# Performance work log

Hardware: AMD Instinct MI355X
Metric: run time of the kernel (lower is better)

The kernel has to match this reference:

```python
import jax, jax.numpy as jnp
import numpy as np
import math

NUM_Q_HEADS = 32
NUM_KV_HEADS = 8


def setup_inputs() -> dict:
    key = jax.random.key(0)
    k1, k2, k3 = jax.random.split(key, 3)
    B, S, E = 2, 2048, 2048
    kv_E = NUM_KV_HEADS * (E // NUM_Q_HEADS)  # 512
    q = jax.random.normal(k1, (B, S, E), dtype=jnp.float32)
    k = jax.random.normal(k2, (B, S, kv_E), dtype=jnp.float32)
    v = jax.random.normal(k3, (B, S, kv_E), dtype=jnp.float32)
    return {"q": q, "k": k, "v": v}


def reference(q, k, v):
    B, S, E = q.shape
    H, KV = NUM_Q_HEADS, NUM_KV_HEADS
    D = E // H
    G = H // KV  # query heads per kv head
    scale = math.sqrt(D)
    # q heads laid out so group g of kv-head h corresponds to q-head h*G+g,
    # matching torch repeat_interleave semantics.
    qh = q.reshape(B, S, KV, G, D).transpose(0, 2, 3, 1, 4)  # [B,KV,G,S,D]
    kh = k.reshape(B, S, KV, D).transpose(0, 2, 1, 3)        # [B,KV,S,D]
    vh = v.reshape(B, S, KV, D).transpose(0, 2, 1, 3)        # [B,KV,S,D]
    scores = jnp.einsum('bkgsd,bktd->bkgst', qh, kh) / scale  # [B,KV,G,S,S]
    weights = jax.nn.softmax(scores, axis=-1)
    out = jnp.einsum('bkgst,bktd->bkgsd', weights, vh)        # [B,KV,G,S,D]
    # back to [B,S,E] with head order (kv_head, group) == q-head index
    return out.transpose(0, 3, 1, 2, 4).reshape(B, S, E)
```

## Files before the change

kernel.cpp:

```cpp
#include <hip/hip_runtime.h>
#include <hip/hip_bf16.h>


#define S_LEN 2048
#define E_DIM 2048
#define KV_E  512
#define D_HEAD 64
#define BN 64
#define NTILE (S_LEN / BN)

typedef __attribute__((ext_vector_type(8))) short short8;
typedef __attribute__((ext_vector_type(4))) float floatx4;

__device__ __forceinline__ short bf(float x) {
    return __builtin_bit_cast(short, __float2bfloat16(x));
}

__global__ __launch_bounds__(256)
void gqa_prepack_kernel(const float* __restrict__ k, const float* __restrict__ v,
                        short* __restrict__ ws) {
    __shared__ float kf[BN][D_HEAD + 2];
    __shared__ float vf[BN][D_HEAD + 2];
    const int kt = blockIdx.x, kvh = blockIdx.y, b = blockIdx.z;
    const int tid = threadIdx.x;
    short* wt = ws + ((size_t)(b * 8 + kvh) * NTILE + kt) * 8192;
    const float* kb = k + ((size_t)(b * S_LEN + kt * BN)) * KV_E + kvh * D_HEAD;
    const float* vb = v + ((size_t)(b * S_LEN + kt * BN)) * KV_E + kvh * D_HEAD;

    #pragma unroll
    for (int i = tid; i < 1024; i += 256) {
        const int r = i >> 4, c0 = (i & 15) << 2;
        floatx4 k4 = *((const floatx4*)(kb + (size_t)r * KV_E + c0));
        floatx4 v4 = *((const floatx4*)(vb + (size_t)r * KV_E + c0));
        kf[r][c0] = k4[0]; kf[r][c0 + 1] = k4[1]; kf[r][c0 + 2] = k4[2]; kf[r][c0 + 3] = k4[3];
        vf[r][c0] = v4[0]; vf[r][c0 + 1] = v4[1]; vf[r][c0 + 2] = v4[2]; vf[r][c0 + 3] = v4[3];
    }
    __syncthreads();
    #pragma unroll
    for (int c = tid; c < 1024; c += 256) {
        const int fk = c >> 6, l = c & 63;
        const int quad = l >> 4, lc = l & 15;
        const int ks = (fk >> 2) & 1, sub = fk & 3;
        short8 s;
        if (fk < 8) {
            const int row = ((lc >> 2) << 3) + (lc & 3) + ((sub & 1) << 2) + ((sub >> 1) << 5);
            const int c0 = ks * 32 + quad * 8;
            #pragma unroll
            for (int j = 0; j < 8; ++j) s[j] = bf(kf[row][c0 + j]);
        } else {
            const int d = sub * 16 + lc;
            const int k0 = ks * 32 + quad * 8;
            #pragma unroll
            for (int j = 0; j < 8; ++j) s[j] = bf(vf[k0 + j][d]);
        }
        *((short8*)(wt + c * 8)) = s;
    }
}

__global__ __launch_bounds__(256, 4)
void GroupedQueryAttention_36163624632989_kernel(
        const float* __restrict__ q,
        const short* __restrict__ ws,
        float* __restrict__ out, const int B) {
    __shared__ short lds[2 * 8192];

    const int f = blockIdx.x;
    const int chunk = gridDim.x >> 3;
    const int wg = (f & 7) * chunk + (f >> 3);
    const int qt = wg & 31;
    const int t2 = wg >> 5;
    const int b  = t2 % B;
    const int hp = t2 / B;
    const int kvh = hp >> 1;

    const int tid  = threadIdx.x;
    const int w    = tid >> 6;
    const int lane = tid & 63;
    const int quad = lane >> 4;
    const int lc   = lane & 15;

    const int h = (hp << 1) + (w & 1);
    const int rowhalf = w >> 1;

    const float SCL = 1.4426950408889634f / 8.0f;

    const short ONE = (short)0x3F80;
    const short8 ones8 = {ONE, ONE, ONE, ONE, ONE, ONE, ONE, ONE};

    short8 aq[2][2];
    #pragma unroll
    for (int mt = 0; mt < 2; ++mt) {
        const int qrow = qt * 64 + rowhalf * 32 + mt * 16 + lc;
        const float* qp = q + ((size_t)(b * S_LEN + qrow)) * E_DIM + h * D_HEAD;
        #pragma unroll
        for (int ks = 0; ks < 2; ++ks) {
            const float* p = qp + ks * 32 + quad * 8;
            floatx4 qa = *((const floatx4*)p);
            floatx4 qb = *((const floatx4*)(p + 4));
            aq[mt][ks][0] = bf(qa[0] * SCL); aq[mt][ks][1] = bf(qa[1] * SCL);
            aq[mt][ks][2] = bf(qa[2] * SCL); aq[mt][ks][3] = bf(qa[3] * SCL);
            aq[mt][ks][4] = bf(qb[0] * SCL); aq[mt][ks][5] = bf(qb[1] * SCL);
            aq[mt][ks][6] = bf(qb[2] * SCL); aq[mt][ks][7] = bf(qb[3] * SCL);
        }
    }

    floatx4 o_acc[2][4];
    floatx4 accL[2];
    #pragma unroll
    for (int mt = 0; mt < 2; ++mt) {
        accL[mt] = (floatx4){0.f, 0.f, 0.f, 0.f};
        #pragma unroll
        for (int i = 0; i < 4; ++i)
            o_acc[mt][i] = (floatx4){0.f, 0.f, 0.f, 0.f};
    }

    const short* wsT = ws + (size_t)(b * 8 + kvh) * NTILE * 8192;

    auto stage = [&](int buf, int kt) {
        const short* src = wsT + (size_t)kt * 8192 + w * 2048 + (lane << 3);
        short* dst = lds + buf * 8192 + w * 2048;
        #pragma unroll
        for (int i = 0; i < 4; ++i)
            __builtin_amdgcn_global_load_lds(
                (const __attribute__((address_space(1))) void*)(src + i * 512),
                (__attribute__((address_space(3))) void*)(dst + i * 512),
                16, 0, 0);
    };

    stage(0, 0);
    __syncthreads();
    int cur = 0;

    for (int kt = 0; kt < NTILE; ++kt) {
        if (kt + 1 < NTILE) stage(cur ^ 1, kt + 1);

        const short* fb = lds + cur * 8192 + (lane << 3);

        floatx4 accT[2][4];
        #pragma unroll
        for (int mt = 0; mt < 2; ++mt)
            #pragma unroll
            for (int t = 0; t < 4; ++t)
                accT[mt][t] = (floatx4){0.f, 0.f, 0.f, 0.f};
        #pragma unroll
        for (int ks = 0; ks < 2; ++ks) {
            short8 bk4[4];
            #pragma unroll
            for (int t = 0; t < 4; ++t)
                bk4[t] = *((const short8*)(fb + (ks * 4 + t) * 512));
            #pragma unroll
            for (int mt = 0; mt < 2; ++mt)
                #pragma unroll
                for (int t = 0; t < 4; ++t)
                    accT[mt][t] = __builtin_amdgcn_mfma_f32_16x16x32_bf16(
                        bk4[t], aq[mt][ks], accT[mt][t], 0, 0, 0);
        }

        #pragma unroll
        for (int ks = 0; ks < 2; ++ks) {
            short8 bv4[4];
            #pragma unroll
            for (int nt = 0; nt < 4; ++nt)
                bv4[nt] = *((const short8*)(fb + (8 + ks * 4 + nt) * 512));
            #pragma unroll
            for (int mt = 0; mt < 2; ++mt) {
                short8 ap;
                #pragma unroll
                for (int r = 0; r < 4; ++r) {
                    ap[r]     = bf(__builtin_amdgcn_exp2f(accT[mt][2 * ks][r]));
                    ap[4 + r] = bf(__builtin_amdgcn_exp2f(accT[mt][2 * ks + 1][r]));
                }
                #pragma unroll
                for (int nt = 0; nt < 4; ++nt)
                    o_acc[mt][nt] = __builtin_amdgcn_mfma_f32_16x16x32_bf16(
                        ap, bv4[nt], o_acc[mt][nt], 0, 0, 0);
                accL[mt] = __builtin_amdgcn_mfma_f32_16x16x32_bf16(
                    ap, ones8, accL[mt], 0, 0, 0);
            }
        }

        __syncthreads();
        cur ^= 1;
    }

    #pragma unroll
    for (int mt = 0; mt < 2; ++mt) {
        float* op = out + (size_t)b * S_LEN * E_DIM + h * D_HEAD;
        #pragma unroll
        for (int r = 0; r < 4; ++r) {
            const float inv_l = 1.0f / accL[mt][r];
            const int grow = qt * 64 + rowhalf * 32 + mt * 16 + quad * 4 + r;
            #pragma unroll
            for (int nt = 0; nt < 4; ++nt)
                op[(size_t)grow * E_DIM + nt * 16 + lc] = o_acc[mt][nt][r] * inv_l;
        }
    }
}

extern "C" void kernel_launch(void* const* d_in, const int* in_sizes, int n_in,
                              void* d_out, int out_size, void* d_ws, size_t ws_size,
                              hipStream_t stream) {
    const float* q = (const float*)d_in[0];
    const float* k = (const float*)d_in[1];
    const float* v = (const float*)d_in[2];
    float* out = (float*)d_out;
    short* ws = (short*)d_ws;
    const int B = in_sizes[0] / (S_LEN * E_DIM);

    dim3 pgrid(NTILE, 8, B);
    gqa_prepack_kernel<<<pgrid, 256, 0, stream>>>(k, v, ws);

    dim3 grid(B * 512);
    GroupedQueryAttention_36163624632989_kernel<<<grid, 256, 0, stream>>>(q, ws, out, B);
}
```

Measured before the change: 155.2 us.

## Halve query and key tile sizes to double grid and occupancy

Shrinks the key tile from 64 to 32 rows and the per-wave query rows from 32 to 16. The prepack layout, LDS staging and MFMA loops are rewritten to match, the grid doubles, and launch bounds now ask for 8 blocks per CU. The aim is more parallelism and occupancy with less register and LDS use per block. In exchange each K/V tile is reused by fewer queries, so global traffic per FLOP roughly doubles, and there are twice as many barrier iterations. The kernel still skips max-subtraction in the softmax (exp2 of raw scaled scores), as before, which relies on input magnitudes staying small.

```diff
diff --git a/kernel.cpp b/kernel.cpp
--- a/kernel.cpp
+++ b/kernel.cpp
@@ -6,8 +6,9 @@
 #define E_DIM 2048
 #define KV_E  512
 #define D_HEAD 64
-#define BN 64
+#define BN 32
 #define NTILE (S_LEN / BN)
+#define TILE_SH 4096
 
 typedef __attribute__((ext_vector_type(8))) short short8;
 typedef __attribute__((ext_vector_type(4))) float floatx4;
@@ -23,12 +24,12 @@
     __shared__ float vf[BN][D_HEAD + 2];
     const int kt = blockIdx.x, kvh = blockIdx.y, b = blockIdx.z;
     const int tid = threadIdx.x;
-    short* wt = ws + ((size_t)(b * 8 + kvh) * NTILE + kt) * 8192;
+    short* wt = ws + ((size_t)(b * 8 + kvh) * NTILE + kt) * TILE_SH;
     const float* kb = k + ((size_t)(b * S_LEN + kt * BN)) * KV_E + kvh * D_HEAD;
     const float* vb = v + ((size_t)(b * S_LEN + kt * BN)) * KV_E + kvh * D_HEAD;
 
     #pragma unroll
-    for (int i = tid; i < 1024; i += 256) {
+    for (int i = tid; i < 512; i += 256) {
         const int r = i >> 4, c0 = (i & 15) << 2;
         floatx4 k4 = *((const floatx4*)(kb + (size_t)r * KV_E + c0));
         floatx4 v4 = *((const floatx4*)(vb + (size_t)r * KV_E + c0));
@@ -37,19 +38,19 @@
     }
     __syncthreads();
     #pragma unroll
-    for (int c = tid; c < 1024; c += 256) {
+    for (int c = tid; c < 512; c += 256) {
         const int fk = c >> 6, l = c & 63;
         const int quad = l >> 4, lc = l & 15;
-        const int ks = (fk >> 2) & 1, sub = fk & 3;
         short8 s;
-        if (fk < 8) {
-            const int row = ((lc >> 2) << 3) + (lc & 3) + ((sub & 1) << 2) + ((sub >> 1) << 5);
+        if (fk < 4) {
+            const int ks = fk >> 1, t = fk & 1;
+            const int row = ((lc >> 2) << 3) + (lc & 3) + (t << 2);
             const int c0 = ks * 32 + quad * 8;
             #pragma unroll
             for (int j = 0; j < 8; ++j) s[j] = bf(kf[row][c0 + j]);
         } else {
-            const int d = sub * 16 + lc;
-            const int k0 = ks * 32 + quad * 8;
+            const int d = (fk - 4) * 16 + lc;
+            const int k0 = quad * 8;
             #pragma unroll
             for (int j = 0; j < 8; ++j) s[j] = bf(vf[k0 + j][d]);
         }
@@ -57,18 +58,18 @@
     }
 }
 
-__global__ __launch_bounds__(256, 4)
+__global__ __launch_bounds__(256, 8)
 void GroupedQueryAttention_36163624632989_kernel(
         const float* __restrict__ q,
         const short* __restrict__ ws,
         float* __restrict__ out, const int B) {
-    __shared__ short lds[2 * 8192];
+    __shared__ short lds[2 * TILE_SH];
 
     const int f = blockIdx.x;
     const int chunk = gridDim.x >> 3;
     const int wg = (f & 7) * chunk + (f >> 3);
-    const int qt = wg & 31;
-    const int t2 = wg >> 5;
+    const int qt = wg & 63;
+    const int t2 = wg >> 6;
     const int b  = t2 % B;
     const int hp = t2 / B;
     const int kvh = hp >> 1;
@@ -87,40 +88,35 @@
     const short ONE = (short)0x3F80;
     const short8 ones8 = {ONE, ONE, ONE, ONE, ONE, ONE, ONE, ONE};
 
-    short8 aq[2][2];
-    #pragma unroll
-    for (int mt = 0; mt < 2; ++mt) {
-        const int qrow = qt * 64 + rowhalf * 32 + mt * 16 + lc;
+    short8 aq[2];
+    {
+        const int qrow = qt * 32 + rowhalf * 16 + lc;
         const float* qp = q + ((size_t)(b * S_LEN + qrow)) * E_DIM + h * D_HEAD;
         #pragma unroll
         for (int ks = 0; ks < 2; ++ks) {
             const float* p = qp + ks * 32 + quad * 8;
             floatx4 qa = *((const floatx4*)p);
             floatx4 qb = *((const floatx4*)(p + 4));
-            aq[mt][ks][0] = bf(qa[0] * SCL); aq[mt][ks][1] = bf(qa[1] * SCL);
-            aq[mt][ks][2] = bf(qa[2] * SCL); aq[mt][ks][3] = bf(qa[3] * SCL);
-            aq[mt][ks][4] = bf(qb[0] * SCL); aq[mt][ks][5] = bf(qb[1] * SCL);
-            aq[mt][ks][6] = bf(qb[2] * SCL); aq[mt][ks][7] = bf(qb[3] * SCL);
+            aq[ks][0] = bf(qa[0] * SCL); aq[ks][1] = bf(qa[1] * SCL);
+            aq[ks][2] = bf(qa[2] * SCL); aq[ks][3] = bf(qa[3] * SCL);
+            aq[ks][4] = bf(qb[0] * SCL); aq[ks][5] = bf(qb[1] * SCL);
+            aq[ks][6] = bf(qb[2] * SCL); aq[ks][7] = bf(qb[3] * SCL);
         }
     }
 
-    floatx4 o_acc[2][4];
-    floatx4 accL[2];
+    floatx4 o_acc[4];
+    floatx4 accL = (floatx4){0.f, 0.f, 0.f, 0.f};
     #pragma unroll
-    for (int mt = 0; mt < 2; ++mt) {
-        accL[mt] = (floatx4){0.f, 0.f, 0.f, 0.f};
-        #pragma unroll
-        for (int i = 0; i < 4; ++i)
-            o_acc[mt][i] = (floatx4){0.f, 0.f, 0.f, 0.f};
-    }
+    for (int i = 0; i < 4; ++i)
+        o_acc[i] = (floatx4){0.f, 0.f, 0.f, 0.f};
 
-    const short* wsT = ws + (size_t)(b * 8 + kvh) * NTILE * 8192;
+    const short* wsT = ws + (size_t)(b * 8 + kvh) * NTILE * TILE_SH;
 
     auto stage = [&](int buf, int kt) {
-        const short* src = wsT + (size_t)kt * 8192 + w * 2048 + (lane << 3);
-        short* dst = lds + buf * 8192 + w * 2048;
+        const short* src = wsT + (size_t)kt * TILE_SH + w * 1024 + (lane << 3);
+        short* dst = lds + buf * TILE_SH + w * 1024;
         #pragma unroll
-        for (int i = 0; i < 4; ++i)
+        for (int i = 0; i < 2; ++i)
             __builtin_amdgcn_global_load_lds(
                 (const __attribute__((address_space(1))) void*)(src + i * 512),
                 (__attribute__((address_space(3))) void*)(dst + i * 512),
@@ -134,65 +130,45 @@
     for (int kt = 0; kt < NTILE; ++kt) {
         if (kt + 1 < NTILE) stage(cur ^ 1, kt + 1);
 
-        const short* fb = lds + cur * 8192 + (lane << 3);
+        const short* fb = lds + cur * TILE_SH + (lane << 3);
 
-        floatx4 accT[2][4];
-        #pragma unroll
-        for (int mt = 0; mt < 2; ++mt)
-            #pragma unroll
-            for (int t = 0; t < 4; ++t)
-                accT[mt][t] = (floatx4){0.f, 0.f, 0.f, 0.f};
+        floatx4 accT[2];
+        accT[0] = (floatx4){0.f, 0.f, 0.f, 0.f};
+        accT[1] = (floatx4){0.f, 0.f, 0.f, 0.f};
         #pragma unroll
         for (int ks = 0; ks < 2; ++ks) {
-            short8 bk4[4];
-            #pragma unroll
-            for (int t = 0; t < 4; ++t)
-                bk4[t] = *((const short8*)(fb + (ks * 4 + t) * 512));
-            #pragma unroll
-            for (int mt = 0; mt < 2; ++mt)
-                #pragma unroll
-                for (int t = 0; t < 4; ++t)
-                    accT[mt][t] = __builtin_amdgcn_mfma_f32_16x16x32_bf16(
-                        bk4[t], aq[mt][ks], accT[mt][t], 0, 0, 0);
+            short8 bk0 = *((const short8*)(fb + (ks * 2 + 0) * 512));
+            short8 bk1 = *((const short8*)(fb + (ks * 2 + 1) * 512));
+            accT[0] = __builtin_amdgcn_mfma_f32_16x16x32_bf16(bk0, aq[ks], accT[0], 0, 0, 0);
+            accT[1] = __builtin_amdgcn_mfma_f32_16x16x32_bf16(bk1, aq[ks], accT[1], 0, 0, 0);
         }
 
+        short8 ap;
         #pragma unroll
-        for (int ks = 0; ks < 2; ++ks) {
-            short8 bv4[4];
-            #pragma unroll
-            for (int nt = 0; nt < 4; ++nt)
-                bv4[nt] = *((const short8*)(fb + (8 + ks * 4 + nt) * 512));
-            #pragma unroll
-            for (int mt = 0; mt < 2; ++mt) {
-                short8 ap;
-                #pragma unroll
-                for (int r = 0; r < 4; ++r) {
-                    ap[r]     = bf(__builtin_amdgcn_exp2f(accT[mt][2 * ks][r]));
-                    ap[4 + r] = bf(__builtin_amdgcn_exp2f(accT[mt][2 * ks + 1][r]));
-                }
-                #pragma unroll
-                for (int nt = 0; nt < 4; ++nt)
-                    o_acc[mt][nt] = __builtin_amdgcn_mfma_f32_16x16x32_bf16(
-                        ap, bv4[nt], o_acc[mt][nt], 0, 0, 0);
-                accL[mt] = __builtin_amdgcn_mfma_f32_16x16x32_bf16(
-                    ap, ones8, accL[mt], 0, 0, 0);
-            }
+        for (int r = 0; r < 4; ++r) {
+            ap[r]     = bf(__builtin_amdgcn_exp2f(accT[0][r]));
+            ap[4 + r] = bf(__builtin_amdgcn_exp2f(accT[1][r]));
         }
+        #pragma unroll
+        for (int nt = 0; nt < 4; ++nt) {
+            short8 bv = *((const short8*)(fb + (4 + nt) * 512));
+            o_acc[nt] = __builtin_amdgcn_mfma_f32_16x16x32_bf16(ap, bv, o_acc[nt], 0, 0, 0);
+        }
+        accL = __builtin_amdgcn_mfma_f32_16x16x32_bf16(ap, ones8, accL, 0, 0, 0);
 
         __syncthreads();
         cur ^= 1;
     }
 
-    #pragma unroll
-    for (int mt = 0; mt < 2; ++mt) {
+    {
         float* op = out + (size_t)b * S_LEN * E_DIM + h * D_HEAD;
         #pragma unroll
         for (int r = 0; r < 4; ++r) {
-            const float inv_l = 1.0f / accL[mt][r];
-            const int grow = qt * 64 + rowhalf * 32 + mt * 16 + quad * 4 + r;
+            const float inv_l = 1.0f / accL[r];
+            const int grow = qt * 32 + rowhalf * 16 + quad * 4 + r;
             #pragma unroll
             for (int nt = 0; nt < 4; ++nt)
-                op[(size_t)grow * E_DIM + nt * 16 + lc] = o_acc[mt][nt][r] * inv_l;
+                op[(size_t)grow * E_DIM + nt * 16 + lc] = o_acc[nt][r] * inv_l;
         }
     }
 }
@@ -210,6 +186,6 @@
     dim3 pgrid(NTILE, 8, B);
     gqa_prepack_kernel<<<pgrid, 256, 0, stream>>>(k, v, ws);
 
-    dim3 grid(B * 512);
+    dim3 grid(B * 1024);
     GroupedQueryAttention_36163624632989_kernel<<<grid, 256, 0, stream>>>(q, ws, out, B);
 }
```

After: 168.4 us. 8.6% more time.

## Split attention waves into producer/consumer roles with LDS-staged probabilities

Applied to the files above, without the earlier changes.

Each workgroup now handles one query head. Its waves are split into producer waves, which compute QK^T and exp and write the probabilities to LDS, and consumer waves, which multiply those probabilities by V one tile later. This is meant to overlap the score/exp phase with the PV MFMA phase. The grid doubles, LDS use grows, and launch bounds drop to 2 blocks per SM. Each wave now does about half the work, and the new LDS round trip for P adds memory traffic and synchronisation.

```diff
diff --git a/kernel.cpp b/kernel.cpp
--- a/kernel.cpp
+++ b/kernel.cpp
@@ -8,6 +8,8 @@
 #define D_HEAD 64
 #define BN 64
 #define NTILE (S_LEN / BN)
+#define VB_OFF 8192
+#define PB_OFF 20480
 
 typedef __attribute__((ext_vector_type(8))) short short8;
 typedef __attribute__((ext_vector_type(4))) float floatx4;
@@ -57,12 +59,12 @@
     }
 }
 
-__global__ __launch_bounds__(256, 4)
+__global__ __launch_bounds__(256, 2)
 void GroupedQueryAttention_36163624632989_kernel(
         const float* __restrict__ q,
         const short* __restrict__ ws,
         float* __restrict__ out, const int B) {
-    __shared__ short lds[2 * 8192];
+    __shared__ short lds[28672];
 
     const int f = blockIdx.x;
     const int chunk = gridDim.x >> 3;
@@ -70,8 +72,8 @@
     const int qt = wg & 31;
     const int t2 = wg >> 5;
     const int b  = t2 % B;
-    const int hp = t2 / B;
-    const int kvh = hp >> 1;
+    const int h  = t2 / B;
+    const int kvh = h >> 2;
 
     const int tid  = threadIdx.x;
     const int w    = tid >> 6;
@@ -79,8 +81,8 @@
     const int quad = lane >> 4;
     const int lc   = lane & 15;
 
-    const int h = (hp << 1) + (w & 1);
-    const int rowhalf = w >> 1;
+    const int pair = w >> 1;
+    const int role = (w ^ f) & 1;
 
     const float SCL = 1.4426950408889634f / 8.0f;
 
@@ -88,19 +90,21 @@
     const short8 ones8 = {ONE, ONE, ONE, ONE, ONE, ONE, ONE, ONE};
 
     short8 aq[2][2];
-    #pragma unroll
-    for (int mt = 0; mt < 2; ++mt) {
-        const int qrow = qt * 64 + rowhalf * 32 + mt * 16 + lc;
-        const float* qp = q + ((size_t)(b * S_LEN + qrow)) * E_DIM + h * D_HEAD;
-        #pragma unroll
-        for (int ks = 0; ks < 2; ++ks) {
-            const float* p = qp + ks * 32 + quad * 8;
-            floatx4 qa = *((const floatx4*)p);
-            floatx4 qb = *((const floatx4*)(p + 4));
-            aq[mt][ks][0] = bf(qa[0] * SCL); aq[mt][ks][1] = bf(qa[1] * SCL);
-            aq[mt][ks][2] = bf(qa[2] * SCL); aq[mt][ks][3] = bf(qa[3] * SCL);
-            aq[mt][ks][4] = bf(qb[0] * SCL); aq[mt][ks][5] = bf(qb[1] * SCL);
-            aq[mt][ks][6] = bf(qb[2] * SCL); aq[mt][ks][7] = bf(qb[3] * SCL);
+    if (role == 0) {
+        #pragma unroll
+        for (int mt = 0; mt < 2; ++mt) {
+            const int qrow = qt * 64 + pair * 32 + mt * 16 + lc;
+            const float* qp = q + ((size_t)(b * S_LEN + qrow)) * E_DIM + h * D_HEAD;
+            #pragma unroll
+            for (int ks = 0; ks < 2; ++ks) {
+                const float* p = qp + ks * 32 + quad * 8;
+                floatx4 qa = *((const floatx4*)p);
+                floatx4 qb = *((const floatx4*)(p + 4));
+                aq[mt][ks][0] = bf(qa[0] * SCL); aq[mt][ks][1] = bf(qa[1] * SCL);
+                aq[mt][ks][2] = bf(qa[2] * SCL); aq[mt][ks][3] = bf(qa[3] * SCL);
+                aq[mt][ks][4] = bf(qb[0] * SCL); aq[mt][ks][5] = bf(qb[1] * SCL);
+                aq[mt][ks][6] = bf(qb[2] * SCL); aq[mt][ks][7] = bf(qb[3] * SCL);
+            }
         }
     }
 
@@ -116,52 +120,49 @@
 
     const short* wsT = ws + (size_t)(b * 8 + kvh) * NTILE * 8192;
 
-    auto stage = [&](int buf, int kt) {
-        const short* src = wsT + (size_t)kt * 8192 + w * 2048 + (lane << 3);
-        short* dst = lds + buf * 8192 + w * 2048;
-        #pragma unroll
-        for (int i = 0; i < 4; ++i)
+    auto stage = [&](int kt) {
+        const short* srcK = wsT + (size_t)kt * 8192 + w * 1024 + (lane << 3);
+        short* dstK = lds + (kt & 1) * 4096 + w * 1024;
+        #pragma unroll
+        for (int i = 0; i < 2; ++i)
             __builtin_amdgcn_global_load_lds(
-                (const __attribute__((address_space(1))) void*)(src + i * 512),
-                (__attribute__((address_space(3))) void*)(dst + i * 512),
+                (const __attribute__((address_space(1))) void*)(srcK + i * 512),
+                (__attribute__((address_space(3))) void*)(dstK + i * 512),
+                16, 0, 0);
+        const short* srcV = wsT + (size_t)kt * 8192 + 4096 + w * 1024 + (lane << 3);
+        short* dstV = lds + VB_OFF + (kt % 3) * 4096 + w * 1024;
+        #pragma unroll
+        for (int i = 0; i < 2; ++i)
+            __builtin_amdgcn_global_load_lds(
+                (const __attribute__((address_space(1))) void*)(srcV + i * 512),
+                (__attribute__((address_space(3))) void*)(dstV + i * 512),
                 16, 0, 0);
     };
 
-    stage(0, 0);
-    __syncthreads();
-    int cur = 0;
-
-    for (int kt = 0; kt < NTILE; ++kt) {
-        if (kt + 1 < NTILE) stage(cur ^ 1, kt + 1);
-
-        const short* fb = lds + cur * 8192 + (lane << 3);
-
+    auto produce = [&](int t) {
+        const short* kb = lds + (t & 1) * 4096 + (lane << 3);
         floatx4 accT[2][4];
         #pragma unroll
         for (int mt = 0; mt < 2; ++mt)
             #pragma unroll
-            for (int t = 0; t < 4; ++t)
-                accT[mt][t] = (floatx4){0.f, 0.f, 0.f, 0.f};
+            for (int t4 = 0; t4 < 4; ++t4)
+                accT[mt][t4] = (floatx4){0.f, 0.f, 0.f, 0.f};
         #pragma unroll
         for (int ks = 0; ks < 2; ++ks) {
             short8 bk4[4];
             #pragma unroll
-            for (int t = 0; t < 4; ++t)
-                bk4[t] = *((const short8*)(fb + (ks * 4 + t) * 512));
+            for (int t4 = 0; t4 < 4; ++t4)
+                bk4[t4] = *((const short8*)(kb + (ks * 4 + t4) * 512));
             #pragma unroll
             for (int mt = 0; mt < 2; ++mt)
                 #pragma unroll
-                for (int t = 0; t < 4; ++t)
-                    accT[mt][t] = __builtin_amdgcn_mfma_f32_16x16x32_bf16(
-                        bk4[t], aq[mt][ks], accT[mt][t], 0, 0, 0);
-        }
-
-        #pragma unroll
-        for (int ks = 0; ks < 2; ++ks) {
-            short8 bv4[4];
-            #pragma unroll
-            for (int nt = 0; nt < 4; ++nt)
-                bv4[nt] = *((const short8*)(fb + (8 + ks * 4 + nt) * 512));
+                for (int t4 = 0; t4 < 4; ++t4)
+                    accT[mt][t4] = __builtin_amdgcn_mfma_f32_16x16x32_bf16(
+                        bk4[t4], aq[mt][ks], accT[mt][t4], 0, 0, 0);
+        }
+        short* pp = lds + PB_OFF + (t & 1) * 4096 + pair * 2048 + (lane << 3);
+        #pragma unroll
+        for (int ks = 0; ks < 2; ++ks)
             #pragma unroll
             for (int mt = 0; mt < 2; ++mt) {
                 short8 ap;
@@ -170,6 +171,22 @@
                     ap[r]     = bf(__builtin_amdgcn_exp2f(accT[mt][2 * ks][r]));
                     ap[4 + r] = bf(__builtin_amdgcn_exp2f(accT[mt][2 * ks + 1][r]));
                 }
+                *((short8*)(pp + (ks * 2 + mt) * 512)) = ap;
+            }
+    };
+
+    auto consume = [&](int u) {
+        const short* vb = lds + VB_OFF + (u % 3) * 4096 + (lane << 3);
+        const short* pb = lds + PB_OFF + (u & 1) * 4096 + pair * 2048 + (lane << 3);
+        #pragma unroll
+        for (int ks = 0; ks < 2; ++ks) {
+            short8 bv4[4];
+            #pragma unroll
+            for (int nt = 0; nt < 4; ++nt)
+                bv4[nt] = *((const short8*)(vb + (ks * 4 + nt) * 512));
+            #pragma unroll
+            for (int mt = 0; mt < 2; ++mt) {
+                short8 ap = *((const short8*)(pb + (ks * 2 + mt) * 512));
                 #pragma unroll
                 for (int nt = 0; nt < 4; ++nt)
                     o_acc[mt][nt] = __builtin_amdgcn_mfma_f32_16x16x32_bf16(
@@ -178,22 +195,30 @@
                     ap, ones8, accL[mt], 0, 0, 0);
             }
         }
-
+    };
+
+    stage(0);
+    __syncthreads();
+    for (int t = 0; t < NTILE; ++t) {
+        if (t + 1 < NTILE) stage(t + 1);
+        if (role == 0) produce(t);
+        else if (t > 0) consume(t - 1);
         __syncthreads();
-        cur ^= 1;
-    }
-
-    #pragma unroll
-    for (int mt = 0; mt < 2; ++mt) {
+    }
+
+    if (role == 1) {
+        consume(NTILE - 1);
         float* op = out + (size_t)b * S_LEN * E_DIM + h * D_HEAD;
         #pragma unroll
-        for (int r = 0; r < 4; ++r) {
-            const float inv_l = 1.0f / accL[mt][r];
-            const int grow = qt * 64 + rowhalf * 32 + mt * 16 + quad * 4 + r;
-            #pragma unroll
-            for (int nt = 0; nt < 4; ++nt)
-                op[(size_t)grow * E_DIM + nt * 16 + lc] = o_acc[mt][nt][r] * inv_l;
-        }
+        for (int mt = 0; mt < 2; ++mt)
+            #pragma unroll
+            for (int r = 0; r < 4; ++r) {
+                const float inv_l = 1.0f / accL[mt][r];
+                const int grow = qt * 64 + pair * 32 + mt * 16 + quad * 4 + r;
+                #pragma unroll
+                for (int nt = 0; nt < 4; ++nt)
+                    op[(size_t)grow * E_DIM + nt * 16 + lc] = o_acc[mt][nt][r] * inv_l;
+            }
     }
 }
 
@@ -210,6 +235,6 @@
     dim3 pgrid(NTILE, 8, B);
     gqa_prepack_kernel<<<pgrid, 256, 0, stream>>>(k, v, ws);
 
-    dim3 grid(B * 512);
+    dim3 grid(B * 1024);
     GroupedQueryAttention_36163624632989_kernel<<<grid, 256, 0, stream>>>(q, ws, out, B);
 }
```

After: 184.8 us. 19.1% more time.
